# Optimization experiments

Hardware: AMD Instinct MI355X
Metric: run time of the kernel (lower is better)

## Reference

```python
import jax, jax.numpy as jnp
import numpy as np
import math

NEG_INF = -1e9  # keras Softmax masking uses a large negative additive constant

def setup_inputs() -> dict:
    key = jax.random.key(0)
    k1, k2, k3, k4 = jax.random.split(key, 4)
    B, T, C, H = 4, 4096, 1024, 128
    x = jax.random.normal(k1, (B, T, C), dtype=jnp.float32)
    Wq = jax.random.normal(k2, (C, H), dtype=jnp.float32) * (1.0 / math.sqrt(C))
    Wk = jax.random.normal(k3, (C, H), dtype=jnp.float32) * (1.0 / math.sqrt(C))
    Wv = jax.random.normal(k4, (C, H), dtype=jnp.float32) * (1.0 / math.sqrt(C))
    return {"x": x, "Wq": Wq, "Wk": Wk, "Wv": Wv}

def reference(x, Wq, Wk, Wv):
    # x: [B, T, C]; projections are bias-free Dense layers
    B, T, C = x.shape
    q = jnp.einsum('btc,ch->bth', x, Wq)  # [B, T, H]
    k = jnp.einsum('btc,ch->bth', x, Wk)  # [B, T, H]
    v = jnp.einsum('btc,ch->bth', x, Wv)  # [B, T, H]
    # NOTE: original scales by sqrt(C) (the input channel dim), not sqrt(head_size)
    wei = jnp.einsum('bth,bsh->bts', q, k) / math.sqrt(C)  # [B, T, T]
    causal = jnp.tril(jnp.ones((T, T), dtype=bool))
    wei = jnp.where(causal[None, :, :], wei, NEG_INF)
    wei = jax.nn.softmax(wei, axis=-1)
    # dropout is identity at inference
    out = jnp.einsum('bts,bsh->bth', wei, v)  # [B, T, H]
    return out
```

## Files before the change

kernel.cpp:

```cpp
#include <hip/hip_runtime.h>
#include <hip/hip_bf16.h>

typedef __bf16 bf16x8 __attribute__((ext_vector_type(8)));
typedef __bf16 bf16x4 __attribute__((ext_vector_type(4)));
typedef float  f32x4  __attribute__((ext_vector_type(4)));

#define NB 4
#define TT 4096
#define CC 1024
#define HH 128
#define PS 72
#define MNEG -30000.0f

__device__ inline void gload16(const void* g, void* l) {
  __builtin_amdgcn_global_load_lds(
      (const __attribute__((address_space(1))) void*)g,
      (__attribute__((address_space(3))) void*)l, 16, 0, 0);
}

__global__ void detect_dtype(const unsigned int* __restrict__ xw, int* __restrict__ flag) {
  int t = threadIdx.x;
  int cnt = 0;
#pragma unroll
  for (int i = 0; i < 4; ++i) {
    unsigned int w = xw[t + 64 * i];
    int e = (int)((w >> 7) & 0xFFu);
    cnt += (e >= 100 && e <= 135) ? 1 : 0;
  }
  cnt += __shfl_xor(cnt, 1);  cnt += __shfl_xor(cnt, 2);  cnt += __shfl_xor(cnt, 4);
  cnt += __shfl_xor(cnt, 8);  cnt += __shfl_xor(cnt, 16); cnt += __shfl_xor(cnt, 32);
  if (t == 0) *flag = (cnt >= 128) ? 1 : 0;
}

__global__ __launch_bounds__(256) void transpose_w3(
    const void* __restrict__ Wq, const void* __restrict__ Wk,
    const void* __restrict__ Wv, __bf16* __restrict__ Wt,
    const int* __restrict__ flagp) {
  int isbf = *flagp;
  int which = blockIdx.y;
  const void* W = (which == 0) ? Wq : (which == 1) ? Wk : Wv;
  int idx = blockIdx.x * 256 + threadIdx.x;
  int h = idx & 127, c = idx >> 7;
  __bf16 val;
  if (isbf) val = ((const __bf16*)W)[c * HH + h];
  else      val = (__bf16)(((const float*)W)[c * HH + h]);
  size_t o = (size_t)(c >> 6) * 24576 + (size_t)which * 8192 +
             (size_t)((c >> 3) & 7) * 1024 + (size_t)h * 8 + (c & 7);
  Wt[o] = val;
}

__global__ __launch_bounds__(768) void qkv_proj(
    const void* __restrict__ x, const __bf16* __restrict__ Wt,
    __bf16* __restrict__ q, __bf16* __restrict__ ktl, __bf16* __restrict__ vtl,
    const int* __restrict__ flagp) {
  __shared__ __align__(16) __bf16 XT[2][4096];
  __shared__ __align__(16) __bf16 WTs[2][24576];
  int isbf = *flagp;
  int tid = threadIdx.x, lane = tid & 63, wave = tid >> 6;
  int which = wave >> 2, rowgrp = wave & 3;
  int l16 = lane & 15, quad = lane >> 4;
  int row0 = blockIdx.x * 64;
  f32x4 acc[8] = {};

#define STAGE(ss, b)                                                          \
  for (int i = wave; i < 56; i += 12) {                                       \
    if (i < 8) {                                                              \
      int row = i * 8 + (lane >> 3), g = lane & 7;                            \
      bf16x8 pk;                                                              \
      if (isbf) {                                                             \
        pk = *(const bf16x8*)((const __bf16*)x + (size_t)(row0 + row) * CC +  \
                              (ss) * 64 + g * 8);                             \
      } else {                                                                \
        const float* xf = (const float*)x + (size_t)(row0 + row) * CC +       \
                          (ss) * 64 + g * 8;                                  \
        f32x4 lo = *(const f32x4*)xf;                                         \
        f32x4 hi = *(const f32x4*)(xf + 4);                                   \
        for (int j = 0; j < 4; ++j) { pk[j] = (__bf16)lo[j]; pk[j+4] = (__bf16)hi[j]; } \
      }                                                                       \
      *(bf16x8*)(&XT[b][g * 512 + (row ^ g) * 8]) = pk;                       \
    } else {                                                                  \
      int j = i - 8;                                                          \
      gload16(Wt + (size_t)(ss) * 24576 + j * 512 + lane * 8,                 \
              &WTs[b][j * 512]);                                              \
    }                                                                         \
  }

  STAGE(0, 0);
  for (int s = 0; s < 16; ++s) {
    int cb = s & 1;
    __syncthreads();
    if (s + 1 < 16) { STAGE(s + 1, cb ^ 1); }
#pragma unroll
    for (int t = 0; t < 2; ++t) {
      int g = t * 4 + quad;
      bf16x8 a = *(const bf16x8*)(&XT[cb][g * 512 + ((rowgrp * 16 + l16) ^ g) * 8]);
#pragma unroll
      for (int nt = 0; nt < 8; ++nt) {
        bf16x8 b = *(const bf16x8*)(&WTs[cb][(size_t)which * 8192 + g * 1024 + (nt * 16 + l16) * 8]);
        acc[nt] = __builtin_amdgcn_mfma_f32_16x16x32_bf16(a, b, acc[nt], 0, 0, 0);
      }
    }
  }
#undef STAGE

  int tile = row0 >> 6;
  if (which == 0) {
#pragma unroll
    for (int nt = 0; nt < 8; ++nt)
#pragma unroll
      for (int r = 0; r < 4; ++r) {
        int row = row0 + rowgrp * 16 + quad * 4 + r;
        q[(size_t)row * HH + nt * 16 + l16] = (__bf16)acc[nt][r];
      }
  } else if (which == 1) {
    __bf16* kb = ktl + (size_t)tile * 8192;
#pragma unroll
    for (int nt = 0; nt < 8; ++nt) {
      int h = nt * 16 + l16, g = h >> 3, j = h & 7;
#pragma unroll
      for (int r = 0; r < 4; ++r) {
        int sidx = rowgrp * 16 + quad * 4 + r;
        kb[g * 512 + sidx * 8 + j] = (__bf16)acc[nt][r];
      }
    }
  } else {
    __bf16* vb = vtl + (size_t)tile * 8192;
#pragma unroll
    for (int nt = 0; nt < 8; ++nt) {
      int h = nt * 16 + l16;
      int sb = rowgrp * 16 + quad * 4;
      bf16x4 pk;
#pragma unroll
      for (int r = 0; r < 4; ++r) pk[r] = (__bf16)acc[nt][r];
      *(bf16x4*)(vb + (sb >> 3) * 1024 + h * 8 + (sb & 7)) = pk;
    }
  }
}

__global__ __launch_bounds__(768, 3) void flash_attn(
    const __bf16* __restrict__ q, const __bf16* __restrict__ ktl,
    const __bf16* __restrict__ vtl, void* __restrict__ out,
    const int* __restrict__ flagp) {
  __shared__ __align__(16) __bf16 PLs[6][2][32 * PS];
  __shared__ float CMB[4][32][132];
  __shared__ float CL[4][32];

  int bx = blockIdx.x;
  int batch = (bx & 7) >> 1;
  int qt0 = ((bx >> 3) << 1) | (bx & 1);

  int tid = threadIdx.x, lane = tid & 63, wave = tid >> 6;
  int p = wave >> 1, rw = wave & 1;
  int l16 = lane & 15, quad = lane >> 4;

  int kA = (6 * (qt0 + 1) + 32) / 65;
  kA = max(1, min(5, kA));
  int qtB = 63 - qt0;
  int unit, kg, nkg, qtu, rbase;
  if (p < kA) { unit = 0; kg = p;      nkg = kA;     qtu = qt0; rbase = 0;  }
  else        { unit = 1; kg = p - kA; nkg = 6 - kA; qtu = qtB; rbase = 32; }

  int qb = qtu * 64;
  int MAXT = max(qt0 / kA + 1, qtB / (6 - kA) + 1);
  int mytrips = (qtu - kg) / nkg + 1;

  const __bf16* qp  = q   + (size_t)batch * TT * HH;
  const __bf16* ktb = ktl + (size_t)batch * TT * HH;
  const __bf16* vtb = vtl + (size_t)batch * TT * HH;

  bf16x8 qf[2][4];
#pragma unroll
  for (int rg = 0; rg < 2; ++rg) {
    const __bf16* qrow = qp + (size_t)(qb + rbase + rg * 16 + l16) * HH + quad * 8;
#pragma unroll
    for (int ks = 0; ks < 4; ++ks) qf[rg][ks] = *(const bf16x8*)(qrow + ks * 32);
  }
  bf16x8 onesf;
#pragma unroll
  for (int j = 0; j < 8; ++j) onesf[j] = (l16 == 0) ? (__bf16)1.0f : (__bf16)0.0f;

  f32x4 acc_o[2][4] = {};
  f32x4 acc_l[2] = {};
  const float SC = 0.0450842200278f;
  const float M0 = 4.0f;

  for (int t = 0; t < MAXT; ++t) {
    int jt = kg + t * nkg;
    int valid = (t < mytrips);
    int jtc = valid ? jt : kg;
    const __bf16* kt  = ktb + (size_t)jtc * 8192;
    const __bf16* vt2 = vtb + (size_t)jtc * 8192;

    bf16x8 kf[4][2];
#pragma unroll
    for (int ks = 0; ks < 4; ++ks)
#pragma unroll
      for (int kn = 0; kn < 2; ++kn)
        kf[ks][kn] = *(const bf16x8*)(kt + ((4 * ks + quad) * 64 + (rw * 2 + kn) * 16 + l16) * 8);

    f32x4 accs[2][2] = {};
#pragma unroll
    for (int ks = 0; ks < 4; ++ks)
#pragma unroll
      for (int rg = 0; rg < 2; ++rg)
#pragma unroll
        for (int kn = 0; kn < 2; ++kn)
          accs[rg][kn] = __builtin_amdgcn_mfma_f32_16x16x32_bf16(qf[rg][ks], kf[ks][kn], accs[rg][kn], 0, 0, 0);

    bf16x8 vf[2][4];
#pragma unroll
    for (int ks2 = 0; ks2 < 2; ++ks2)
#pragma unroll
      for (int nt = 0; nt < 4; ++nt)
        vf[ks2][nt] = *(const bf16x8*)(vt2 + (ks2 * 4 + quad) * 1024 + (rw * 64 + nt * 16 + l16) * 8);

    float pv[2][2][4];
    if (valid && jt == qtu) {
#pragma unroll
      for (int rg = 0; rg < 2; ++rg)
#pragma unroll
        for (int kn = 0; kn < 2; ++kn) {
          int kcol = jt * 64 + (rw * 2 + kn) * 16 + l16;
          int qr0 = qb + rbase + rg * 16 + quad * 4;
#pragma unroll
          for (int r = 0; r < 4; ++r) {
            float z = fmaf(accs[rg][kn][r], SC, -M0);
            z = (kcol <= qr0 + r) ? z : MNEG;
            pv[rg][kn][r] = exp2f(z);
          }
        }
    } else if (valid) {
#pragma unroll
      for (int rg = 0; rg < 2; ++rg)
#pragma unroll
        for (int kn = 0; kn < 2; ++kn)
#pragma unroll
          for (int r = 0; r < 4; ++r)
            pv[rg][kn][r] = exp2f(fmaf(accs[rg][kn][r], SC, -M0));
    } else {
#pragma unroll
      for (int rg = 0; rg < 2; ++rg)
#pragma unroll
        for (int kn = 0; kn < 2; ++kn)
#pragma unroll
          for (int r = 0; r < 4; ++r)
            pv[rg][kn][r] = 0.0f;
    }

    __bf16* pw = &PLs[p][t & 1][0];
#pragma unroll
    for (int rg = 0; rg < 2; ++rg)
#pragma unroll
      for (int kn = 0; kn < 2; ++kn)
#pragma unroll
        for (int r = 0; r < 4; ++r)
          pw[(rg * 16 + quad * 4 + r) * PS + (rw * 2 + kn) * 16 + l16] = (__bf16)pv[rg][kn][r];

    __syncthreads();

#pragma unroll
    for (int ks2 = 0; ks2 < 2; ++ks2) {
      bf16x8 pa0 = *(const bf16x8*)(pw + l16 * PS + ks2 * 32 + quad * 8);
      bf16x8 pa1 = *(const bf16x8*)(pw + (16 + l16) * PS + ks2 * 32 + quad * 8);
      acc_l[0] = __builtin_amdgcn_mfma_f32_16x16x32_bf16(pa0, onesf, acc_l[0], 0, 0, 0);
      acc_l[1] = __builtin_amdgcn_mfma_f32_16x16x32_bf16(pa1, onesf, acc_l[1], 0, 0, 0);
#pragma unroll
      for (int nt = 0; nt < 4; ++nt) {
        acc_o[0][nt] = __builtin_amdgcn_mfma_f32_16x16x32_bf16(pa0, vf[ks2][nt], acc_o[0][nt], 0, 0, 0);
        acc_o[1][nt] = __builtin_amdgcn_mfma_f32_16x16x32_bf16(pa1, vf[ks2][nt], acc_o[1][nt], 0, 0, 0);
      }
    }
  }

  if (kg > 0) {
    int slot = (unit == 0) ? (kg - 1) : (kA - 1 + kg - 1);
#pragma unroll
    for (int rh = 0; rh < 2; ++rh)
#pragma unroll
      for (int nt = 0; nt < 4; ++nt)
#pragma unroll
        for (int r = 0; r < 4; ++r)
          CMB[slot][rh * 16 + quad * 4 + r][rw * 64 + nt * 16 + l16] = acc_o[rh][nt][r];
    if (rw == 0 && l16 == 0) {
#pragma unroll
      for (int rh = 0; rh < 2; ++rh)
#pragma unroll
        for (int r = 0; r < 4; ++r) CL[slot][rh * 16 + quad * 4 + r] = acc_l[rh][r];
    }
  }
  __syncthreads();
  if (kg == 0) {
    int lo  = (unit == 0) ? 0 : kA - 1;
    int cnt = (unit == 0) ? kA - 1 : 5 - kA;
    int isbf = *flagp;
    __bf16* ob = (__bf16*)out + (size_t)batch * TT * HH;
    float*  of = (float*)out  + (size_t)batch * TT * HH;
#pragma unroll
    for (int rh = 0; rh < 2; ++rh) {
      float inv[4];
#pragma unroll
      for (int r = 0; r < 4; ++r) {
        float lr = __shfl(acc_l[rh][r], lane & 48);
        for (int c = 0; c < cnt; ++c) lr += CL[lo + c][rh * 16 + quad * 4 + r];
        inv[r] = 1.f / fmaxf(lr, 1e-30f);
      }
#pragma unroll
      for (int nt = 0; nt < 4; ++nt)
#pragma unroll
        for (int r = 0; r < 4; ++r) {
          int row = qb + rbase + rh * 16 + quad * 4 + r;
          int col = rw * 64 + nt * 16 + l16;
          float val = acc_o[rh][nt][r];
          for (int c = 0; c < cnt; ++c) val += CMB[lo + c][rh * 16 + quad * 4 + r][col];
          val *= inv[r];
          size_t idx = (size_t)row * HH + col;
          if (isbf) ob[idx] = (__bf16)val;
          else      of[idx] = val;
        }
    }
  }
}

extern "C" void kernel_launch(void* const* d_in, const int* in_sizes, int n_in,
                              void* d_out, int out_size, void* d_ws, size_t ws_size,
                              hipStream_t stream) {
  const void* x  = d_in[0];
  const void* Wq = d_in[1];
  const void* Wk = d_in[2];
  const void* Wv = d_in[3];
  char* wsb = (char*)d_ws;
  __bf16* q   = (__bf16*)wsb;
  __bf16* ktl = q   + (size_t)NB * TT * HH;
  __bf16* vtl = ktl + (size_t)NB * TT * HH;
  __bf16* wt  = vtl + (size_t)NB * TT * HH;
  size_t base = (((size_t)(3 * NB * TT * HH + 3 * CC * HH) * 2) + 255) & ~(size_t)255;
  int* flag = (int*)(wsb + base);
  (void)ws_size; (void)in_sizes; (void)n_in; (void)out_size;

  detect_dtype<<<1, 64, 0, stream>>>((const unsigned int*)x, flag);
  transpose_w3<<<dim3(512, 3), 256, 0, stream>>>(Wq, Wk, Wv, wt, flag);
  qkv_proj<<<256, 768, 0, stream>>>(x, wt, q, ktl, vtl, flag);
  flash_attn<<<NB * 64, 768, 0, stream>>>(q, ktl, vtl, d_out, flag);
}
```

Before: 173.6 us.

## Prefetch next K/V tiles into registers, inline dtype probe, lighten barrier

Removes the separate dtype-detection kernel launch. Each kernel now probes the input bits itself with a per-wave check, which saves one launch and its dependency. In flash attention, the K and V fragments for the next key tile are loaded one iteration ahead into registers, so global load latency overlaps the MFMA and softmax work. The __syncthreads is replaced by an LDS-only waitcnt plus s_barrier, so the barrier no longer waits on the outstanding global prefetches. The cost is higher register pressure and redundant probe reads in every block.

```diff
diff --git a/kernel.cpp b/kernel.cpp
--- a/kernel.cpp
+++ b/kernel.cpp
@@ -18,25 +18,25 @@
       (__attribute__((address_space(3))) void*)l, 16, 0, 0);
 }
 
-__global__ void detect_dtype(const unsigned int* __restrict__ xw, int* __restrict__ flag) {
-  int t = threadIdx.x;
+__device__ __forceinline__ int probe_isbf(const unsigned int* __restrict__ xw) {
+  int lane = threadIdx.x & 63;
   int cnt = 0;
 #pragma unroll
   for (int i = 0; i < 4; ++i) {
-    unsigned int w = xw[t + 64 * i];
+    unsigned int w = xw[lane + 64 * i];
     int e = (int)((w >> 7) & 0xFFu);
     cnt += (e >= 100 && e <= 135) ? 1 : 0;
   }
   cnt += __shfl_xor(cnt, 1);  cnt += __shfl_xor(cnt, 2);  cnt += __shfl_xor(cnt, 4);
   cnt += __shfl_xor(cnt, 8);  cnt += __shfl_xor(cnt, 16); cnt += __shfl_xor(cnt, 32);
-  if (t == 0) *flag = (cnt >= 128) ? 1 : 0;
+  return cnt >= 128;
 }
 
 __global__ __launch_bounds__(256) void transpose_w3(
     const void* __restrict__ Wq, const void* __restrict__ Wk,
     const void* __restrict__ Wv, __bf16* __restrict__ Wt,
-    const int* __restrict__ flagp) {
-  int isbf = *flagp;
+    const unsigned int* __restrict__ xw) {
+  int isbf = probe_isbf(xw);
   int which = blockIdx.y;
   const void* W = (which == 0) ? Wq : (which == 1) ? Wk : Wv;
   int idx = blockIdx.x * 256 + threadIdx.x;
@@ -51,11 +51,10 @@
 
 __global__ __launch_bounds__(768) void qkv_proj(
     const void* __restrict__ x, const __bf16* __restrict__ Wt,
-    __bf16* __restrict__ q, __bf16* __restrict__ ktl, __bf16* __restrict__ vtl,
-    const int* __restrict__ flagp) {
+    __bf16* __restrict__ q, __bf16* __restrict__ ktl, __bf16* __restrict__ vtl) {
   __shared__ __align__(16) __bf16 XT[2][4096];
   __shared__ __align__(16) __bf16 WTs[2][24576];
-  int isbf = *flagp;
+  int isbf = probe_isbf((const unsigned int*)x);
   int tid = threadIdx.x, lane = tid & 63, wave = tid >> 6;
   int which = wave >> 2, rowgrp = wave & 3;
   int l16 = lane & 15, quad = lane >> 4;
@@ -140,7 +139,7 @@
 __global__ __launch_bounds__(768, 3) void flash_attn(
     const __bf16* __restrict__ q, const __bf16* __restrict__ ktl,
     const __bf16* __restrict__ vtl, void* __restrict__ out,
-    const int* __restrict__ flagp) {
+    const unsigned int* __restrict__ xw) {
   __shared__ __align__(16) __bf16 PLs[6][2][32 * PS];
   __shared__ float CMB[4][32][132];
   __shared__ float CL[4][32];
@@ -164,6 +163,8 @@
   int MAXT = max(qt0 / kA + 1, qtB / (6 - kA) + 1);
   int mytrips = (qtu - kg) / nkg + 1;
 
+  int isbf = probe_isbf(xw);
+
   const __bf16* qp  = q   + (size_t)batch * TT * HH;
   const __bf16* ktb = ktl + (size_t)batch * TT * HH;
   const __bf16* vtb = vtl + (size_t)batch * TT * HH;
@@ -184,19 +185,27 @@
   const float SC = 0.0450842200278f;
   const float M0 = 4.0f;
 
+  bf16x8 kf[4][2];
+  bf16x8 vf[2][4];
+  {
+    const __bf16* kt0 = ktb + (size_t)kg * 8192;
+#pragma unroll
+    for (int ks = 0; ks < 4; ++ks)
+#pragma unroll
+      for (int kn = 0; kn < 2; ++kn)
+        kf[ks][kn] = *(const bf16x8*)(kt0 + ((4 * ks + quad) * 64 + (rw * 2 + kn) * 16 + l16) * 8);
+    const __bf16* vt0 = vtb + (size_t)kg * 8192;
+#pragma unroll
+    for (int ks2 = 0; ks2 < 2; ++ks2)
+#pragma unroll
+      for (int nt = 0; nt < 4; ++nt)
+        vf[ks2][nt] = *(const bf16x8*)(vt0 + (ks2 * 4 + quad) * 1024 + (rw * 64 + nt * 16 + l16) * 8);
+  }
+
   for (int t = 0; t < MAXT; ++t) {
     int jt = kg + t * nkg;
     int valid = (t < mytrips);
-    int jtc = valid ? jt : kg;
-    const __bf16* kt  = ktb + (size_t)jtc * 8192;
-    const __bf16* vt2 = vtb + (size_t)jtc * 8192;
-
-    bf16x8 kf[4][2];
-#pragma unroll
-    for (int ks = 0; ks < 4; ++ks)
-#pragma unroll
-      for (int kn = 0; kn < 2; ++kn)
-        kf[ks][kn] = *(const bf16x8*)(kt + ((4 * ks + quad) * 64 + (rw * 2 + kn) * 16 + l16) * 8);
+    int jn = (t + 1 < mytrips) ? (kg + (t + 1) * nkg) : kg;
 
     f32x4 accs[2][2] = {};
 #pragma unroll
@@ -207,12 +216,14 @@
         for (int kn = 0; kn < 2; ++kn)
           accs[rg][kn] = __builtin_amdgcn_mfma_f32_16x16x32_bf16(qf[rg][ks], kf[ks][kn], accs[rg][kn], 0, 0, 0);
 
-    bf16x8 vf[2][4];
-#pragma unroll
-    for (int ks2 = 0; ks2 < 2; ++ks2)
-#pragma unroll
-      for (int nt = 0; nt < 4; ++nt)
-        vf[ks2][nt] = *(const bf16x8*)(vt2 + (ks2 * 4 + quad) * 1024 + (rw * 64 + nt * 16 + l16) * 8);
+    {
+      const __bf16* ktn = ktb + (size_t)jn * 8192;
+#pragma unroll
+      for (int ks = 0; ks < 4; ++ks)
+#pragma unroll
+        for (int kn = 0; kn < 2; ++kn)
+          kf[ks][kn] = *(const bf16x8*)(ktn + ((4 * ks + quad) * 64 + (rw * 2 + kn) * 16 + l16) * 8);
+    }
 
     float pv[2][2][4];
     if (valid && jt == qtu) {
@@ -256,7 +267,9 @@
         for (int r = 0; r < 4; ++r)
           pw[(rg * 16 + quad * 4 + r) * PS + (rw * 2 + kn) * 16 + l16] = (__bf16)pv[rg][kn][r];
 
-    __syncthreads();
+    asm volatile("s_waitcnt lgkmcnt(0)" ::: "memory");
+    __builtin_amdgcn_s_barrier();
+    __builtin_amdgcn_sched_barrier(0);
 
 #pragma unroll
     for (int ks2 = 0; ks2 < 2; ++ks2) {
@@ -270,6 +283,15 @@
         acc_o[1][nt] = __builtin_amdgcn_mfma_f32_16x16x32_bf16(pa1, vf[ks2][nt], acc_o[1][nt], 0, 0, 0);
       }
     }
+
+    {
+      const __bf16* vtn = vtb + (size_t)jn * 8192;
+#pragma unroll
+      for (int ks2 = 0; ks2 < 2; ++ks2)
+#pragma unroll
+        for (int nt = 0; nt < 4; ++nt)
+          vf[ks2][nt] = *(const bf16x8*)(vtn + (ks2 * 4 + quad) * 1024 + (rw * 64 + nt * 16 + l16) * 8);
+    }
   }
 
   if (kg > 0) {
@@ -292,7 +314,6 @@
   if (kg == 0) {
     int lo  = (unit == 0) ? 0 : kA - 1;
     int cnt = (unit == 0) ? kA - 1 : 5 - kA;
-    int isbf = *flagp;
     __bf16* ob = (__bf16*)out + (size_t)batch * TT * HH;
     float*  of = (float*)out  + (size_t)batch * TT * HH;
 #pragma unroll
@@ -333,12 +354,11 @@
   __bf16* ktl = q   + (size_t)NB * TT * HH;
   __bf16* vtl = ktl + (size_t)NB * TT * HH;
   __bf16* wt  = vtl + (size_t)NB * TT * HH;
-  size_t base = (((size_t)(3 * NB * TT * HH + 3 * CC * HH) * 2) + 255) & ~(size_t)255;
-  int* flag = (int*)(wsb + base);
   (void)ws_size; (void)in_sizes; (void)n_in; (void)out_size;
 
-  detect_dtype<<<1, 64, 0, stream>>>((const unsigned int*)x, flag);
-  transpose_w3<<<dim3(512, 3), 256, 0, stream>>>(Wq, Wk, Wv, wt, flag);
-  qkv_proj<<<256, 768, 0, stream>>>(x, wt, q, ktl, vtl, flag);
-  flash_attn<<<NB * 64, 768, 0, stream>>>(q, ktl, vtl, d_out, flag);
-}
+  transpose_w3<<<dim3(512, 3), 256, 0, stream>>>(Wq, Wk, Wv, wt,
+                                                 (const unsigned int*)x);
+  qkv_proj<<<256, 768, 0, stream>>>(x, wt, q, ktl, vtl);
+  flash_attn<<<NB * 64, 768, 0, stream>>>(q, ktl, vtl, d_out,
+                                          (const unsigned int*)x);
+}
```

Measured after the change: 250.3 us. 44.2% more time.
